# Performance work log

Measured on AMD Instinct MI355X. Metric: run time of the kernel, lower is better.

Reference implementation:

```python
import jax, jax.numpy as jnp
import numpy as np

HEADS = 8
DIM_HEAD = 64
WINDOW = 512
SCALE = DIM_HEAD ** -0.5


def setup_inputs() -> dict:
    key = jax.random.key(0)
    k1, k2, k3 = jax.random.split(key, 3)
    b, dim, n = 2, 256, 32768
    hidden = HEADS * DIM_HEAD  # 512
    x = jax.random.normal(k1, (b, dim, n), dtype=jnp.float32)
    # Conv1d(dim, hidden*3, 1, bias=False) weight -> [3*hidden, dim]
    w_qkv = jax.random.normal(k2, (3 * hidden, dim), dtype=jnp.float32) * (dim ** -0.5)
    # Conv1d(hidden, dim, 1) weight/bias
    w_out = jax.random.normal(k3, (dim, hidden), dtype=jnp.float32) * (hidden ** -0.5)
    b_out = jnp.zeros((dim,), dtype=jnp.float32)
    return {"x": x, "w_qkv": w_qkv, "w_out": w_out, "b_out": b_out}


def reference(x, w_qkv, w_out, b_out):
    b, c, n = x.shape
    h, d, w = HEADS, DIM_HEAD, WINDOW
    nw = n // w  # n chosen divisible by window size
    # 1x1 conv == channel matmul
    qkv = jnp.einsum('oc,bcn->bon', w_qkv, x)  # [b, 3*h*d, n]
    q, k, v = jnp.split(qkv, 3, axis=1)
    # [b, h, d, nw, w]
    def to_windows(t):
        return t.reshape(b, h, d, nw, w)
    q = to_windows(q) * SCALE
    k = to_windows(k)
    v = to_windows(v)
    # non-overlapping local windows: block-diagonal attention
    sim = jnp.einsum('bhdni,bhdnj->bhnij', q, k)        # [b,h,nw,w,w]
    attn = jax.nn.softmax(sim, axis=-1)
    out = jnp.einsum('bhnij,bhdnj->bhdni', attn, v)      # [b,h,d,nw,w]
    out = out.reshape(b, h * d, n)
    return jnp.einsum('oc,bcn->bon', w_out, out) + b_out[None, :, None]
```

## Files before the change

### kernel.cpp

```cpp
#include <hip/hip_runtime.h>
#include <stdint.h>
#include <stddef.h>


typedef _Float16 f16;
typedef _Float16 half8 __attribute__((ext_vector_type(8)));
typedef float f32x4 __attribute__((ext_vector_type(4)));

#define NSEQ 32768
#define NTOT 65536
#define WIN  512

__device__ __forceinline__ void async_copy16(const f16* g, f16* l) {
  __builtin_amdgcn_global_load_lds(
      (const __attribute__((address_space(1))) void*)g,
      (__attribute__((address_space(3))) void*)l, 16, 0, 0);
}

__device__ __forceinline__ int packrtz(float a, float b) {
  typedef __fp16 fp16v2 __attribute__((ext_vector_type(2)));
  fp16v2 h = __builtin_amdgcn_cvt_pkrtz(a, b);
  return __builtin_bit_cast(int, h);
}

__global__ __launch_bounds__(256) void convert_w(
    const float* __restrict__ wqkv, const float* __restrict__ wout,
    f16* __restrict__ wqh, f16* __restrict__ woh) {
  int idx = blockIdx.x * 256 + threadIdx.x;
  if (idx < 1536 * 256) {
    float v = wqkv[idx];
    if (idx < 512 * 256) v *= 0.18033688011112042f;
    wqh[idx] = (f16)v;
  } else {
    int j = idx - 1536 * 256;
    if (j < 256 * 512) woh[j] = (f16)wout[j];
  }
}

__global__ __launch_bounds__(256) void transpose_x(
    const float* __restrict__ x, f16* __restrict__ xT) {
  __shared__ alignas(16) float tile[32][33];
  const int tx = threadIdx.x & 31, ty = threadIdx.x >> 5;
  const int bx = blockIdx.x, by = blockIdx.y;
  const float* xb = x + (size_t)blockIdx.z * 256 * NSEQ;
  f16* xTb = xT + (size_t)blockIdx.z * NSEQ * 256;
#pragma unroll
  for (int r = 0; r < 4; ++r) {
    int c = by * 32 + ty + r * 8;
    int n = bx * 32 + tx;
    tile[ty + r * 8][tx] = xb[(size_t)c * NSEQ + n];
  }
  __syncthreads();
  const int tx16 = threadIdx.x & 15, ty16 = threadIdx.x >> 4;
#pragma unroll
  for (int r = 0; r < 2; ++r) {
    int n = bx * 32 + ty16 + r * 16;
    int c = by * 32 + tx16 * 2;
    union {
      f16 h[2];
      int i;
    } u;
    u.h[0] = (f16)tile[tx16 * 2][ty16 + r * 16];
    u.h[1] = (f16)tile[tx16 * 2 + 1][ty16 + r * 16];
    *(int*)(xTb + (size_t)n * 256 + c) = u.i;
  }
}

template <int MODE, int SWZ>
__global__ __launch_bounds__(256) void gemm_k(
    const f16* __restrict__ A, const f16* __restrict__ Bm,
    void* __restrict__ outp, const float* __restrict__ bias, int K,
    int bstride, int ostride) {
  __shared__ alignas(16) f16 As[3][4096];
  __shared__ alignas(16) f16 Bs[3][4096];
  const int tid = threadIdx.x;
  const int lane = tid & 63, wid = tid >> 6;
  const int quad = lane >> 4, lid = lane & 15;

  int colb, rowb;
  if (SWZ) {
    int lin = blockIdx.y * 8 + blockIdx.x;
    int x = lin & 7, s = lin >> 3;
    colb = s & 7;
    rowb = x * 64 + (s >> 3);
  } else {
    colb = blockIdx.x;
    rowb = blockIdx.y;
  }
  const int row0 = rowb * 128, col0 = colb * 128;
  const int wm = (wid >> 1) * 64, wn = (wid & 1) * 64;

  f32x4 acc[4][4];
  const f32x4 zero = {0.f, 0.f, 0.f, 0.f};
#pragma unroll
  for (int i = 0; i < 4; ++i)
#pragma unroll
    for (int j = 0; j < 4; ++j) acc[i][j] = zero;

  const int kIters = K >> 5;

  auto stage = [&](int kt, int buf) {
    const int k0 = kt * 32;
#pragma unroll
    for (int rd = 0; rd < 2; ++rd) {
      int slot = rd * 256 + tid;
      int r = slot & 127, kc = slot >> 7;
      async_copy16(A + (size_t)(row0 + r) * K + k0 + kc * 8,
                   &As[buf][slot * 8]);
      async_copy16(Bm + (size_t)(col0 + r) * bstride + k0 + kc * 8,
                   &Bs[buf][slot * 8]);
    }
  };

  stage(0, 0);
  stage(1, 1);
  for (int kt = 0; kt < kIters; ++kt) {
    const int pb = kt % 3;
    asm volatile("s_waitcnt lgkmcnt(0)" ::: "memory");
    __builtin_amdgcn_sched_barrier(0);
    __builtin_amdgcn_s_barrier();
    __builtin_amdgcn_sched_barrier(0);
    if (kt + 2 < kIters) {
      stage(kt + 2, (kt + 2) % 3);
      asm volatile("s_waitcnt vmcnt(8)" ::: "memory");
    } else if (kt + 1 < kIters) {
      asm volatile("s_waitcnt vmcnt(4)" ::: "memory");
    } else {
      asm volatile("s_waitcnt vmcnt(0)" ::: "memory");
    }
    __builtin_amdgcn_sched_barrier(0);
    __builtin_amdgcn_s_barrier();
    __builtin_amdgcn_sched_barrier(0);

    half8 af[4], bf[4];
#pragma unroll
    for (int mi = 0; mi < 4; ++mi)
      af[mi] = *(const half8*)(&As[pb][(quad * 128 + wm + mi * 16 + lid) * 8]);
#pragma unroll
    for (int ni = 0; ni < 4; ++ni)
      bf[ni] = *(const half8*)(&Bs[pb][(quad * 128 + wn + ni * 16 + lid) * 8]);
#pragma unroll
    for (int mi = 0; mi < 4; ++mi)
#pragma unroll
      for (int ni = 0; ni < 4; ++ni)
        acc[mi][ni] = __builtin_amdgcn_mfma_f32_16x16x32_f16(
            af[mi], bf[ni], acc[mi][ni], 0, 0, 0);
  }

#pragma unroll
  for (int mi = 0; mi < 4; ++mi) {
#pragma unroll
    for (int r = 0; r < 4; ++r) {
      int grow = row0 + wm + mi * 16 + quad * 4 + r;
#pragma unroll
      for (int ni = 0; ni < 4; ++ni) {
        int gcol = col0 + wn + ni * 16 + lid;
        float v = acc[mi][ni][r];
        if (MODE == 2) {
          ((float*)outp)[(size_t)(gcol >> 15) * (256u * 32768u) +
                         (size_t)grow * 32768 + (gcol & 32767)] =
              v + bias[grow];
        } else {
          ((f16*)outp)[(size_t)grow * ostride + gcol] = (f16)v;
        }
      }
    }
  }
}

__global__ __launch_bounds__(512, 2) void attn_k(
    const f16* __restrict__ qk, const f16* __restrict__ vws,
    f16* __restrict__ ows) {
  __shared__ alignas(16) f16 smem[24576];

  const int tid = threadIdx.x;
  const int lane = tid & 63, wid = tid >> 6;
  const int quad = lane >> 4, lid = lane & 15;
  const int win = blockIdx.x;
  const int h = blockIdx.y;
  const size_t nbase = (size_t)blockIdx.z * NSEQ + (size_t)win * WIN;
  const int iw0 = wid * 64;

  half8 aq[4][2];
#pragma unroll
  for (int ig = 0; ig < 4; ++ig)
#pragma unroll
    for (int ks = 0; ks < 2; ++ks)
      aq[ig][ks] = *(const half8*)(qk + (nbase + iw0 + ig * 16 + lid) * 1024 +
                                   h * 64 + ks * 32 + quad * 8);

  f32x4 OT[4][4];
  const f32x4 zero = {0.f, 0.f, 0.f, 0.f};
#pragma unroll
  for (int di = 0; di < 4; ++di)
#pragma unroll
    for (int ig = 0; ig < 4; ++ig) OT[di][ig] = zero;
  float l_run[4] = {0.f, 0.f, 0.f, 0.f};

  const int sa = tid & 63, sc = tid >> 6;
  const int psa = (sa & 32) | ((sa & 12) << 1) | ((sa >> 2) & 4) | (sa & 3);

  auto stage = [&](int jt) {
    f16* Kb = smem + (jt % 3) * 8192;
    const int j0 = jt * 64;
    async_copy16(qk + (nbase + j0 + psa) * 1024 + 512 + h * 64 + sc * 8,
                 Kb + tid * 8);
    async_copy16(vws + (size_t)(h * 64 + sa) * NTOT + nbase + j0 + sc * 8,
                 Kb + 4096 + tid * 8);
  };

  stage(0);
  stage(1);

  for (int jt = 0; jt < 8; ++jt) {
    const int pb = jt % 3;
    asm volatile("s_waitcnt lgkmcnt(0)" ::: "memory");
    __builtin_amdgcn_sched_barrier(0);
    __builtin_amdgcn_s_barrier();
    __builtin_amdgcn_sched_barrier(0);
    if (jt + 2 < 8) {
      stage(jt + 2);
      asm volatile("s_waitcnt vmcnt(4)" ::: "memory");
    } else if (jt + 1 < 8) {
      asm volatile("s_waitcnt vmcnt(2)" ::: "memory");
    } else {
      asm volatile("s_waitcnt vmcnt(0)" ::: "memory");
    }
    __builtin_amdgcn_sched_barrier(0);
    __builtin_amdgcn_s_barrier();
    __builtin_amdgcn_sched_barrier(0);

    const f16* Ks = smem + pb * 8192;
    const f16* Vs = smem + pb * 8192 + 4096;

    f32x4 sT[4][4];
#pragma unroll
    for (int jg = 0; jg < 4; ++jg)
#pragma unroll
      for (int ig = 0; ig < 4; ++ig) sT[jg][ig] = zero;
    __builtin_amdgcn_s_setprio(1);
#pragma unroll
    for (int ks = 0; ks < 2; ++ks)
#pragma unroll
      for (int jg = 0; jg < 4; ++jg) {
        half8 bk =
            *(const half8*)(Ks + ((ks * 4 + quad) * 64 + jg * 16 + lid) * 8);
#pragma unroll
        for (int ig = 0; ig < 4; ++ig)
          sT[jg][ig] = __builtin_amdgcn_mfma_f32_16x16x32_f16(
              bk, aq[ig][ks], sT[jg][ig], 0, 0, 0);
      }
    __builtin_amdgcn_s_setprio(0);

    int pk[4][4][2];
#pragma unroll
    for (int jg = 0; jg < 4; ++jg)
#pragma unroll
      for (int ig = 0; ig < 4; ++ig) {
        float e0 = __builtin_amdgcn_exp2f(sT[jg][ig][0]);
        float e1 = __builtin_amdgcn_exp2f(sT[jg][ig][1]);
        float e2 = __builtin_amdgcn_exp2f(sT[jg][ig][2]);
        float e3 = __builtin_amdgcn_exp2f(sT[jg][ig][3]);
        l_run[ig] += (e0 + e1) + (e2 + e3);
        pk[jg][ig][0] = packrtz(e0, e1);
        pk[jg][ig][1] = packrtz(e2, e3);
      }

    __builtin_amdgcn_s_setprio(1);
#pragma unroll
    for (int ks2 = 0; ks2 < 2; ++ks2) {
      const int ta = ks2 * 2, tb = ta + 1;
      half8 pt[4];
#pragma unroll
      for (int ig = 0; ig < 4; ++ig) {
        union {
          int i[4];
          half8 h;
        } u;
        u.i[0] = pk[ta][ig][0];
        u.i[1] = pk[ta][ig][1];
        u.i[2] = pk[tb][ig][0];
        u.i[3] = pk[tb][ig][1];
        pt[ig] = u.h;
      }
#pragma unroll
      for (int di = 0; di < 4; ++di) {
        half8 av =
            *(const half8*)(Vs + ((ks2 * 4 + quad) * 64 + di * 16 + lid) * 8);
#pragma unroll
        for (int ig = 0; ig < 4; ++ig)
          OT[di][ig] = __builtin_amdgcn_mfma_f32_16x16x32_f16(
              av, pt[ig], OT[di][ig], 0, 0, 0);
      }
    }
    __builtin_amdgcn_s_setprio(0);
  }

#pragma unroll
  for (int ig = 0; ig < 4; ++ig) {
    l_run[ig] += __shfl_xor(l_run[ig], 16, 64);
    l_run[ig] += __shfl_xor(l_run[ig], 32, 64);
  }

#pragma unroll
  for (int ig = 0; ig < 4; ++ig) {
    float inv = 1.0f / l_run[ig];
    size_t rowb = (nbase + iw0 + ig * 16 + lid) * 1024 + h * 64;
#pragma unroll
    for (int di = 0; di < 4; ++di) {
      int2 o;
      o.x = packrtz(OT[di][ig][0] * inv, OT[di][ig][1] * inv);
      o.y = packrtz(OT[di][ig][2] * inv, OT[di][ig][3] * inv);
      *(int2*)(ows + rowb + di * 16 + quad * 4) = o;
    }
  }
}

extern "C" void kernel_launch(void* const* d_in, const int* in_sizes, int n_in,
                              void* d_out, int out_size, void* d_ws,
                              size_t ws_size, hipStream_t stream) {
  const float* x = (const float*)d_in[0];
  const float* w_qkv = (const float*)d_in[1];
  const float* w_out = (const float*)d_in[2];
  const float* b_out = (const float*)d_in[3];

  char* ws = (char*)d_ws;
  f16* qkw = (f16*)(ws);
  f16* vw = (f16*)(ws + 134217728);
  f16* xT = (f16*)(ws + 201326592);
  f16* wqh = (f16*)(ws + 234881024);
  f16* woh = (f16*)(ws + 235667456);

  convert_w<<<2048, 256, 0, stream>>>(w_qkv, w_out, wqh, woh);
  transpose_x<<<dim3(1024, 8, 2), 256, 0, stream>>>(x, xT);
  gemm_k<0, 1><<<dim3(8, 512), 256, 0, stream>>>(xT, wqh, qkw, nullptr, 256,
                                                 256, 1024);
  gemm_k<0, 0><<<dim3(512, 4), 256, 0, stream>>>(wqh + 1024 * 256, xT, vw,
                                                 nullptr, 256, 256, NTOT);
  attn_k<<<dim3(64, 8, 2), 512, 0, stream>>>(qkw, vw, qkw);
  gemm_k<2, 0><<<dim3(512, 2), 256, 0, stream>>>(woh, qkw, d_out, b_out, 512,
                                                 1024, 0);
}
```

Baseline: 395.3 us.

## Quad-buffer K/V tiles and synchronize once per pair of tiles

The attention loop moves from a triple-buffered ring with two barriers per 64-key tile to four LDS buffers. Two tiles are staged per superstep behind a single __syncthreads, which cuts barrier and waitcnt stalls in half. Loads also get a whole two-tile superstep to land before they are consumed. In exchange, LDS per block grows from 48KB to 64KB, and the inner tile loop is no longer unrolled.

New measurement: 406.7 us. 2.9% more time.

```diff
diff --git a/kernel.cpp b/kernel.cpp
--- a/kernel.cpp
+++ b/kernel.cpp
@@ -171,7 +171,7 @@
 __global__ __launch_bounds__(512, 2) void attn_k(
     const f16* __restrict__ qk, const f16* __restrict__ vws,
     f16* __restrict__ ows) {
-  __shared__ alignas(16) f16 smem[24576];
+  __shared__ alignas(16) f16 smem[32768];
 
   const int tid = threadIdx.x;
   const int lane = tid & 63, wid = tid >> 6;
@@ -201,7 +201,7 @@
   const int psa = (sa & 32) | ((sa & 12) << 1) | ((sa >> 2) & 4) | (sa & 3);
 
   auto stage = [&](int jt) {
-    f16* Kb = smem + (jt % 3) * 8192;
+    f16* Kb = smem + (jt & 3) * 8192;
     const int j0 = jt * 64;
     async_copy16(qk + (nbase + j0 + psa) * 1024 + 512 + h * 64 + sc * 8,
                  Kb + tid * 8);
@@ -212,88 +212,80 @@
   stage(0);
   stage(1);
 
-  for (int jt = 0; jt < 8; ++jt) {
-    const int pb = jt % 3;
-    asm volatile("s_waitcnt lgkmcnt(0)" ::: "memory");
-    __builtin_amdgcn_sched_barrier(0);
-    __builtin_amdgcn_s_barrier();
-    __builtin_amdgcn_sched_barrier(0);
-    if (jt + 2 < 8) {
-      stage(jt + 2);
-      asm volatile("s_waitcnt vmcnt(4)" ::: "memory");
-    } else if (jt + 1 < 8) {
-      asm volatile("s_waitcnt vmcnt(2)" ::: "memory");
-    } else {
-      asm volatile("s_waitcnt vmcnt(0)" ::: "memory");
-    }
-    __builtin_amdgcn_sched_barrier(0);
-    __builtin_amdgcn_s_barrier();
-    __builtin_amdgcn_sched_barrier(0);
-
-    const f16* Ks = smem + pb * 8192;
-    const f16* Vs = smem + pb * 8192 + 4096;
-
-    f32x4 sT[4][4];
-#pragma unroll
-    for (int jg = 0; jg < 4; ++jg)
-#pragma unroll
-      for (int ig = 0; ig < 4; ++ig) sT[jg][ig] = zero;
-    __builtin_amdgcn_s_setprio(1);
-#pragma unroll
-    for (int ks = 0; ks < 2; ++ks)
-#pragma unroll
-      for (int jg = 0; jg < 4; ++jg) {
-        half8 bk =
-            *(const half8*)(Ks + ((ks * 4 + quad) * 64 + jg * 16 + lid) * 8);
-#pragma unroll
-        for (int ig = 0; ig < 4; ++ig)
-          sT[jg][ig] = __builtin_amdgcn_mfma_f32_16x16x32_f16(
-              bk, aq[ig][ks], sT[jg][ig], 0, 0, 0);
+  for (int s = 0; s < 4; ++s) {
+    __syncthreads();
+    if (s < 3) {
+      stage(2 * s + 2);
+      stage(2 * s + 3);
+    }
+#pragma unroll 1
+    for (int t = 0; t < 2; ++t) {
+      const int jt = 2 * s + t;
+      const f16* Ks = smem + (jt & 3) * 8192;
+      const f16* Vs = Ks + 4096;
+
+      f32x4 sT[4][4];
+#pragma unroll
+      for (int jg = 0; jg < 4; ++jg)
+#pragma unroll
+        for (int ig = 0; ig < 4; ++ig) sT[jg][ig] = zero;
+      __builtin_amdgcn_s_setprio(1);
+#pragma unroll
+      for (int ks = 0; ks < 2; ++ks)
+#pragma unroll
+        for (int jg = 0; jg < 4; ++jg) {
+          half8 bk =
+              *(const half8*)(Ks + ((ks * 4 + quad) * 64 + jg * 16 + lid) * 8);
+#pragma unroll
+          for (int ig = 0; ig < 4; ++ig)
+            sT[jg][ig] = __builtin_amdgcn_mfma_f32_16x16x32_f16(
+                bk, aq[ig][ks], sT[jg][ig], 0, 0, 0);
+        }
+      __builtin_amdgcn_s_setprio(0);
+
+      int pk[4][4][2];
+#pragma unroll
+      for (int jg = 0; jg < 4; ++jg)
+#pragma unroll
+        for (int ig = 0; ig < 4; ++ig) {
+          float e0 = __builtin_amdgcn_exp2f(sT[jg][ig][0]);
+          float e1 = __builtin_amdgcn_exp2f(sT[jg][ig][1]);
+          float e2 = __builtin_amdgcn_exp2f(sT[jg][ig][2]);
+          float e3 = __builtin_amdgcn_exp2f(sT[jg][ig][3]);
+          l_run[ig] += (e0 + e1) + (e2 + e3);
+          pk[jg][ig][0] = packrtz(e0, e1);
+          pk[jg][ig][1] = packrtz(e2, e3);
+        }
+
+      __builtin_amdgcn_s_setprio(1);
+#pragma unroll
+      for (int ks2 = 0; ks2 < 2; ++ks2) {
+        const int ta = ks2 * 2, tb = ta + 1;
+        half8 pt[4];
+#pragma unroll
+        for (int ig = 0; ig < 4; ++ig) {
+          union {
+            int i[4];
+            half8 h;
+          } u;
+          u.i[0] = pk[ta][ig][0];
+          u.i[1] = pk[ta][ig][1];
+          u.i[2] = pk[tb][ig][0];
+          u.i[3] = pk[tb][ig][1];
+          pt[ig] = u.h;
+        }
+#pragma unroll
+        for (int di = 0; di < 4; ++di) {
+          half8 av = *(const half8*)(Vs +
+                                     ((ks2 * 4 + quad) * 64 + di * 16 + lid) * 8);
+#pragma unroll
+          for (int ig = 0; ig < 4; ++ig)
+            OT[di][ig] = __builtin_amdgcn_mfma_f32_16x16x32_f16(
+                av, pt[ig], OT[di][ig], 0, 0, 0);
+        }
       }
-    __builtin_amdgcn_s_setprio(0);
-
-    int pk[4][4][2];
-#pragma unroll
-    for (int jg = 0; jg < 4; ++jg)
-#pragma unroll
-      for (int ig = 0; ig < 4; ++ig) {
-        float e0 = __builtin_amdgcn_exp2f(sT[jg][ig][0]);
-        float e1 = __builtin_amdgcn_exp2f(sT[jg][ig][1]);
-        float e2 = __builtin_amdgcn_exp2f(sT[jg][ig][2]);
-        float e3 = __builtin_amdgcn_exp2f(sT[jg][ig][3]);
-        l_run[ig] += (e0 + e1) + (e2 + e3);
-        pk[jg][ig][0] = packrtz(e0, e1);
-        pk[jg][ig][1] = packrtz(e2, e3);
-      }
-
-    __builtin_amdgcn_s_setprio(1);
-#pragma unroll
-    for (int ks2 = 0; ks2 < 2; ++ks2) {
-      const int ta = ks2 * 2, tb = ta + 1;
-      half8 pt[4];
-#pragma unroll
-      for (int ig = 0; ig < 4; ++ig) {
-        union {
-          int i[4];
-          half8 h;
-        } u;
-        u.i[0] = pk[ta][ig][0];
-        u.i[1] = pk[ta][ig][1];
-        u.i[2] = pk[tb][ig][0];
-        u.i[3] = pk[tb][ig][1];
-        pt[ig] = u.h;
-      }
-#pragma unroll
-      for (int di = 0; di < 4; ++di) {
-        half8 av =
-            *(const half8*)(Vs + ((ks2 * 4 + quad) * 64 + di * 16 + lid) * 8);
-#pragma unroll
-        for (int ig = 0; ig < 4; ++ig)
-          OT[di][ig] = __builtin_amdgcn_mfma_f32_16x16x32_f16(
-              av, pt[ig], OT[di][ig], 0, 0, 0);
-      }
-    }
-    __builtin_amdgcn_s_setprio(0);
+      __builtin_amdgcn_s_setprio(0);
+    }
   }
 
 #pragma unroll
```
